# Kernel tuning notes

Measured on AMD Instinct MI355X. Metric: run time of the kernel, lower is better.

Reference implementation:

```python
import math
import jax, jax.numpy as jnp
import numpy as np

TEMPERATURE = 1.0
N_SAMPLES = 7
B, D = 2048, 512

def _l2_normalize(x, eps=1e-12):
    return x / jnp.maximum(jnp.linalg.norm(x, axis=-1, keepdims=True), eps)

def setup_inputs() -> dict:
    key = jax.random.key(0)
    ks = jax.random.split(key, 7)
    return {
        "query_mean": jax.random.normal(ks[0], (B, D), jnp.float32),
        "query_logsigma": jax.random.normal(ks[1], (B, D), jnp.float32),
        "query_z": jax.random.normal(ks[2], (B,), jnp.float32),
        "target_mean": jax.random.normal(ks[3], (B, D), jnp.float32),
        "target_logsigma": jax.random.normal(ks[4], (B, D), jnp.float32),
        "target_z": jax.random.normal(ks[5], (B,), jnp.float32),
        "eps": jax.random.normal(ks[6], (B, N_SAMPLES, D), jnp.float32),
    }

def reference(query_mean, query_logsigma, query_z, target_mean, target_logsigma, target_z, eps):
    qm = _l2_normalize(query_mean)                       # [B, D]
    tm = _l2_normalize(target_mean)                      # [B, D]
    # sample_gaussian_tensors: mu + eps * exp(logsigma), 7 samples -> [B, 7, D]
    samples = tm[:, None, :] + eps * jnp.exp(target_logsigma)[:, None, :]
    inv_sigmas = jnp.exp(-query_logsigma)                # [B, D] per-query precisions
    # weighted squared distance via the GEMM trick:
    # sum_d (t - q)^2 * w = sum_d t^2 w - 2 sum_d t q w + sum_d q^2 w
    t_term = jnp.einsum('qd,tsd->qts', inv_sigmas, samples * samples)   # [Bq, Bt, 7]
    x_term = jnp.einsum('qd,tsd->qts', qm * inv_sigmas, samples)        # [Bq, Bt, 7]
    q_term = jnp.sum(qm * qm * inv_sigmas, axis=-1)                     # [Bq]
    sqdist = t_term - 2.0 * x_term + q_term[:, None, None]
    loc = -0.5 * jnp.mean(sqdist, axis=-1)                              # [Bq, Bt]
    d = qm.shape[-1]
    norm_constant = (-d / 2.0) * jnp.log(jnp.float32(2.0 * math.pi)) \
                    - 0.5 * jnp.sum(query_logsigma, axis=-1)            # [Bq]
    # NOTE: torch broadcasting aligns the [B] vectors to the LAST (target) axis
    scores = query_z + norm_constant + loc                              # [Bq, Bt]
    scores = scores - jnp.max(scores, axis=0, keepdims=True)
    logits = scores / TEMPERATURE
    logp = jax.nn.log_softmax(logits, axis=-1)
    idx = jnp.arange(scores.shape[0])
    loss = -jnp.mean(logp[idx, idx])                                    # reduction='mean'
    return loss

if __name__ == "__main__":
    print(reference(**setup_inputs()))
```

## Files before the change

kernel.cpp:

```cpp
#include <hip/hip_runtime.h>
#include <math.h>

#define BB 2048
#define DD 512
#define NS 7
#define KK 1024
#define BM 128
#define BN 64
#define BK 64
#define NT (KK / BK)

typedef __attribute__((ext_vector_type(8))) short short8;
typedef __attribute__((ext_vector_type(4))) float floatx4;

typedef const __attribute__((address_space(1))) void gv_t;
typedef __attribute__((address_space(3))) void lv_t;
__device__ __forceinline__ void gl2lds16(const void* g, void* l) {
  __builtin_amdgcn_global_load_lds((gv_t*)g, (lv_t*)l, 16, 0, 0);
}

__device__ __forceinline__ unsigned short f2bf(float f) {
  unsigned int u = __float_as_uint(f);
  u += 0x7FFFu + ((u >> 16) & 1u);
  return (unsigned short)(u >> 16);
}
__device__ __forceinline__ float bf2f(unsigned short u) {
  return __uint_as_float(((unsigned)u) << 16);
}

__device__ __forceinline__ unsigned fkey(float f) {
  unsigned u = __float_as_uint(f);
  return (u & 0x80000000u) ? ~u : (u | 0x80000000u);
}
__device__ __forceinline__ float funkey(unsigned k) {
  unsigned u = (k & 0x80000000u) ? (k ^ 0x80000000u) : ~k;
  return __uint_as_float(u);
}

__device__ __forceinline__ int swz(int row, int c) {
  return (c & ~0x38) | ((((c >> 3) ^ row) & 7) << 3);
}

__device__ __forceinline__ float wave_reduce_sum(float v) {
#pragma unroll
  for (int off = 32; off > 0; off >>= 1) v += __shfl_down(v, off, 64);
  return v;
}
__device__ __forceinline__ float wave_reduce_max(float v) {
#pragma unroll
  for (int off = 32; off > 0; off >>= 1) v = fmaxf(v, __shfl_down(v, off, 64));
  return v;
}
__device__ __forceinline__ float block_reduce_sum256(float v, float* sbuf) {
  v = wave_reduce_sum(v);
  if ((threadIdx.x & 63) == 0) sbuf[threadIdx.x >> 6] = v;
  __syncthreads();
  float r = sbuf[0] + sbuf[1] + sbuf[2] + sbuf[3];
  __syncthreads();
  return r;
}
__device__ __forceinline__ float block_reduce_max256(float v, float* sbuf) {
  v = wave_reduce_max(v);
  if ((threadIdx.x & 63) == 0) sbuf[threadIdx.x >> 6] = v;
  __syncthreads();
  float r = fmaxf(fmaxf(sbuf[0], sbuf[1]), fmaxf(sbuf[2], sbuf[3]));
  __syncthreads();
  return r;
}

__global__ __launch_bounds__(256) void prep(
    const float* __restrict__ qmean, const float* __restrict__ qls,
    const float* __restrict__ tmean, const float* __restrict__ tls,
    const float* __restrict__ eps,
    unsigned short* __restrict__ Acat, unsigned short* __restrict__ Bcat,
    float* __restrict__ qterm, unsigned* __restrict__ Mkey) {
  __shared__ float sbuf[4];
  const int b = blockIdx.x, tid = threadIdx.x;
  const int c0 = 2 * tid;
  if (b < BB) {
    const int q = b;
    float2 x = ((const float2*)(qmean + (size_t)q * DD))[tid];
    float2 l = ((const float2*)(qls + (size_t)q * DD))[tid];
    float ss = block_reduce_sum256(x.x * x.x + x.y * x.y, sbuf);
    float inv = 1.0f / fmaxf(sqrtf(ss), 1e-12f);
    float w0 = expf(-l.x), w1 = expf(-l.y);
    float n0 = x.x * inv, n1 = x.y * inv;
    unsigned short* arow = Acat + (size_t)q * KK;
    ushort2 wp, np;
    wp.x = f2bf(w0);             wp.y = f2bf(w1);
    np.x = f2bf(-2.0f * n0 * w0); np.y = f2bf(-2.0f * n1 * w1);
    *(ushort2*)&arow[swz(q, c0)]      = wp;
    *(ushort2*)&arow[swz(q, DD + c0)] = np;
    float qt = block_reduce_sum256(n0 * n0 * w0 + n1 * n1 * w1, sbuf);
    if (tid == 0) qterm[q] = qt;
  } else {
    const int t = b - BB;
    if (tid == 0) Mkey[t] = 0u;
    float2 x = ((const float2*)(tmean + (size_t)t * DD))[tid];
    float2 l = ((const float2*)(tls + (size_t)t * DD))[tid];
    float ss = block_reduce_sum256(x.x * x.x + x.y * x.y, sbuf);
    float inv = 1.0f / fmaxf(sqrtf(ss), 1e-12f);
    float tm0 = x.x * inv, tm1 = x.y * inv;
    float sg0 = expf(l.x), sg1 = expf(l.y);
    float se0 = 0.f, sq0 = 0.f, se1 = 0.f, sq1 = 0.f;
    const float2* ep = (const float2*)(eps + (size_t)t * NS * DD);
#pragma unroll
    for (int s = 0; s < NS; ++s) {
      float2 e = ep[s * (DD / 2) + tid];
      se0 += e.x; sq0 += e.x * e.x;
      se1 += e.y; sq1 += e.y * e.y;
    }
    const float i7 = 1.0f / 7.0f;
    float m0 = sg0 * se0 * i7, m1 = sg1 * se1 * i7;
    unsigned short* brow = Bcat + (size_t)t * KK;
    ushort2 s2p, s1p;
    s2p.x = f2bf(tm0 * tm0 + 2.0f * tm0 * m0 + sg0 * sg0 * sq0 * i7);
    s2p.y = f2bf(tm1 * tm1 + 2.0f * tm1 * m1 + sg1 * sg1 * sq1 * i7);
    s1p.x = f2bf(tm0 + m0); s1p.y = f2bf(tm1 + m1);
    *(ushort2*)&brow[swz(t, c0)]      = s2p;
    *(ushort2*)&brow[swz(t, DD + c0)] = s1p;
  }
}

__global__ __launch_bounds__(256) void gemm_loc(
    const unsigned short* __restrict__ Acat,
    const unsigned short* __restrict__ Bcat,
    const float* __restrict__ qterm,
    unsigned short* __restrict__ loc, unsigned* __restrict__ Mkey) {
  __shared__ short As[3][BM * BK];
  __shared__ short Bs[3][BN * BK];
  const int tid = threadIdx.x, lane = tid & 63, wid = tid >> 6;
  const int lin = blockIdx.y * (BB / BN) + blockIdx.x;
  const int xcd = lin & 7, j = lin >> 3;
  const int tr = ((xcd >> 2) << 3) + (j >> 3);
  const int tc = ((xcd & 3) << 3) + (j & 7);
  const int brow = tr * BM, bcol = tc * BN;
  const int wr = wid >> 1, wc = wid & 1;
  const int fr = lane & 15, kg = lane >> 4, f7 = fr & 7;
  const int srow = lane >> 3, scol = (lane & 7) * 8;

  floatx4 acc[4][2];
#pragma unroll
  for (int m = 0; m < 4; ++m)
#pragma unroll
    for (int n = 0; n < 2; ++n) acc[m][n] = (floatx4){0.f, 0.f, 0.f, 0.f};

  const unsigned short* gA = Acat + (size_t)(brow + wid * 32 + srow) * KK + scol;
  const unsigned short* gB = Bcat + (size_t)(bcol + wid * 16 + srow) * KK + scol;

#pragma unroll
  for (int p = 0; p < 2; ++p) {
    short* la = &As[p][wid * 2048];
    short* lb = &Bs[p][wid * 1024];
#pragma unroll
    for (int j2 = 0; j2 < 4; ++j2) gl2lds16(gA + (size_t)j2 * 8 * KK + p * BK, la + j2 * 512);
#pragma unroll
    for (int j2 = 0; j2 < 2; ++j2) gl2lds16(gB + (size_t)j2 * 8 * KK + p * BK, lb + j2 * 512);
  }

#pragma unroll
  for (int kt = 0; kt < NT; ++kt) {
    if (kt < NT - 1) asm volatile("s_waitcnt vmcnt(6)" ::: "memory");
    else             asm volatile("s_waitcnt vmcnt(0)" ::: "memory");
    __builtin_amdgcn_s_barrier();
    if (kt + 2 < NT) {
      const int kc = (kt + 2) * BK, nb = (kt + 2) % 3;
      short* la = &As[nb][wid * 2048];
      short* lb = &Bs[nb][wid * 1024];
#pragma unroll
      for (int j2 = 0; j2 < 4; ++j2) gl2lds16(gA + (size_t)j2 * 8 * KK + kc, la + j2 * 512);
#pragma unroll
      for (int j2 = 0; j2 < 2; ++j2) gl2lds16(gB + (size_t)j2 * 8 * KK + kc, lb + j2 * 512);
    }
    const short* a  = As[kt % 3];
    const short* bp = Bs[kt % 3];
#pragma unroll
    for (int kh = 0; kh < 2; ++kh) {
      const int co = (((kh * 4 + kg) ^ f7) << 3);
      short8 af[4], bf[2];
#pragma unroll
      for (int m = 0; m < 4; ++m)
        af[m] = *reinterpret_cast<const short8*>(&a[(wr * 64 + m * 16 + fr) * BK + co]);
#pragma unroll
      for (int n = 0; n < 2; ++n)
        bf[n] = *reinterpret_cast<const short8*>(&bp[(wc * 32 + n * 16 + fr) * BK + co]);
#pragma unroll
      for (int m = 0; m < 4; ++m)
#pragma unroll
        for (int n = 0; n < 2; ++n)
          acc[m][n] = __builtin_amdgcn_mfma_f32_16x16x32_bf16(af[m], bf[n],
                                                              acc[m][n], 0, 0, 0);
    }
  }

#pragma unroll
  for (int n = 0; n < 2; ++n) {
    const int col = bcol + wc * 32 + n * 16 + fr;
    float cm = -3.402823466e38f;
#pragma unroll
    for (int m = 0; m < 4; ++m) {
      const int row = brow + wr * 64 + m * 16 + kg * 4;
#pragma unroll
      for (int r4 = 0; r4 < 4; ++r4) {
        float v = -0.5f * (acc[m][n][r4] + qterm[row + r4]);
        loc[(size_t)(row + r4) * BB + col] = f2bf(v);
        cm = fmaxf(cm, v);
      }
    }
    cm = fmaxf(cm, __shfl_xor(cm, 16, 64));
    cm = fmaxf(cm, __shfl_xor(cm, 32, 64));
    if (kg == 0) atomicMax(&Mkey[col], fkey(cm));
  }
}

__global__ __launch_bounds__(256) void row_lse(
    const unsigned short* __restrict__ loc, const unsigned* __restrict__ Mkey,
    float* __restrict__ rowval) {
  __shared__ float sbuf[4];
  __shared__ float sdiag;
  const int q = blockIdx.x, tid = threadIdx.x;
  short8 v = ((const short8*)(loc + (size_t)q * BB))[tid];
  uint4 k0 = ((const uint4*)Mkey)[2 * tid];
  uint4 k1 = ((const uint4*)Mkey)[2 * tid + 1];
  float xs[8];
  xs[0] = bf2f((unsigned short)v[0]) - funkey(k0.x);
  xs[1] = bf2f((unsigned short)v[1]) - funkey(k0.y);
  xs[2] = bf2f((unsigned short)v[2]) - funkey(k0.z);
  xs[3] = bf2f((unsigned short)v[3]) - funkey(k0.w);
  xs[4] = bf2f((unsigned short)v[4]) - funkey(k1.x);
  xs[5] = bf2f((unsigned short)v[5]) - funkey(k1.y);
  xs[6] = bf2f((unsigned short)v[6]) - funkey(k1.z);
  xs[7] = bf2f((unsigned short)v[7]) - funkey(k1.w);
  float m = xs[0];
#pragma unroll
  for (int i = 1; i < 8; ++i) m = fmaxf(m, xs[i]);
  if ((q >> 3) == tid) sdiag = xs[q & 7];
  m = block_reduce_max256(m, sbuf);
  float s = 0.f;
#pragma unroll
  for (int i = 0; i < 8; ++i) s += expf(xs[i] - m);
  s = block_reduce_sum256(s, sbuf);
  if (tid == 0) rowval[q] = sdiag - (m + logf(s));
}

__global__ __launch_bounds__(256) void final_loss(
    const float* __restrict__ rowval, float* __restrict__ out) {
  __shared__ float sbuf[4];
  const int tid = threadIdx.x;
  float s = 0.f;
#pragma unroll
  for (int i = 0; i < 8; ++i) s += rowval[tid + i * 256];
  s = block_reduce_sum256(s, sbuf);
  if (tid == 0) out[0] = -s * (1.0f / (float)BB);
}

extern "C" void kernel_launch(void* const* d_in, const int* in_sizes, int n_in,
                              void* d_out, int out_size, void* d_ws, size_t ws_size,
                              hipStream_t stream) {
  const float* qmean = (const float*)d_in[0];
  const float* qls   = (const float*)d_in[1];
  const float* tmean = (const float*)d_in[3];
  const float* tls   = (const float*)d_in[4];
  const float* eps   = (const float*)d_in[6];

  char* ws = (char*)d_ws;
  unsigned short* Acat = (unsigned short*)(ws + 0);
  unsigned short* Bcat = (unsigned short*)(ws + (4u << 20));
  float* qterm         = (float*)(ws + (8u << 20));
  unsigned* Mkey       = (unsigned*)(ws + (8u << 20) + 8192);
  float* rowval        = (float*)(ws + (8u << 20) + 16384);
  unsigned short* loc  = (unsigned short*)(ws + (8u << 20) + 65536);

  prep<<<2 * BB, 256, 0, stream>>>(qmean, qls, tmean, tls, eps,
                                   Acat, Bcat, qterm, Mkey);
  gemm_loc<<<dim3(BB / BN, BB / BM), 256, 0, stream>>>(Acat, Bcat, qterm, loc, Mkey);
  row_lse<<<BB, 256, 0, stream>>>(loc, Mkey, rowval);
  final_loss<<<1, 256, 0, stream>>>(rowval, (float*)d_out);
}
```

Before: 38.76 us.

## Switch GEMM operands to FP8 with split-scaled accumulators and wave-per-row prep/lse

```diff
diff --git a/kernel.cpp b/kernel.cpp
--- a/kernel.cpp
+++ b/kernel.cpp
@@ -12,6 +12,7 @@
 
 typedef __attribute__((ext_vector_type(8))) short short8;
 typedef __attribute__((ext_vector_type(4))) float floatx4;
+typedef long long i64;
 
 typedef const __attribute__((address_space(1))) void gv_t;
 typedef __attribute__((address_space(3))) void lv_t;
@@ -37,98 +38,121 @@
   return __uint_as_float(u);
 }
 
-__device__ __forceinline__ int swz(int row, int c) {
-  return (c & ~0x38) | ((((c >> 3) ^ row) & 7) << 3);
-}
-
-__device__ __forceinline__ float wave_reduce_sum(float v) {
-#pragma unroll
-  for (int off = 32; off > 0; off >>= 1) v += __shfl_down(v, off, 64);
+__device__ __forceinline__ uint2 pack8_fp8(const float* v) {
+  int lo = 0, hi = 0;
+  lo = __builtin_amdgcn_cvt_pk_fp8_f32(v[0], v[1], lo, false);
+  lo = __builtin_amdgcn_cvt_pk_fp8_f32(v[2], v[3], lo, true);
+  hi = __builtin_amdgcn_cvt_pk_fp8_f32(v[4], v[5], hi, false);
+  hi = __builtin_amdgcn_cvt_pk_fp8_f32(v[6], v[7], hi, true);
+  uint2 r; r.x = (unsigned)lo; r.y = (unsigned)hi; return r;
+}
+
+
+__device__ __forceinline__ float wsum(float v) {
+#pragma unroll
+  for (int off = 32; off > 0; off >>= 1) v += __shfl_xor(v, off, 64);
   return v;
 }
-__device__ __forceinline__ float wave_reduce_max(float v) {
-#pragma unroll
-  for (int off = 32; off > 0; off >>= 1) v = fmaxf(v, __shfl_down(v, off, 64));
+__device__ __forceinline__ float wmax(float v) {
+#pragma unroll
+  for (int off = 32; off > 0; off >>= 1) v = fmaxf(v, __shfl_xor(v, off, 64));
   return v;
 }
 __device__ __forceinline__ float block_reduce_sum256(float v, float* sbuf) {
-  v = wave_reduce_sum(v);
+  v = wsum(v);
   if ((threadIdx.x & 63) == 0) sbuf[threadIdx.x >> 6] = v;
   __syncthreads();
   float r = sbuf[0] + sbuf[1] + sbuf[2] + sbuf[3];
   __syncthreads();
   return r;
 }
-__device__ __forceinline__ float block_reduce_max256(float v, float* sbuf) {
-  v = wave_reduce_max(v);
-  if ((threadIdx.x & 63) == 0) sbuf[threadIdx.x >> 6] = v;
-  __syncthreads();
-  float r = fmaxf(fmaxf(sbuf[0], sbuf[1]), fmaxf(sbuf[2], sbuf[3]));
-  __syncthreads();
-  return r;
-}
 
 __global__ __launch_bounds__(256) void prep(
     const float* __restrict__ qmean, const float* __restrict__ qls,
     const float* __restrict__ tmean, const float* __restrict__ tls,
     const float* __restrict__ eps,
-    unsigned short* __restrict__ Acat, unsigned short* __restrict__ Bcat,
+    unsigned char* __restrict__ Acat, unsigned char* __restrict__ Bcat,
     float* __restrict__ qterm, unsigned* __restrict__ Mkey) {
-  __shared__ float sbuf[4];
-  const int b = blockIdx.x, tid = threadIdx.x;
-  const int c0 = 2 * tid;
-  if (b < BB) {
-    const int q = b;
-    float2 x = ((const float2*)(qmean + (size_t)q * DD))[tid];
-    float2 l = ((const float2*)(qls + (size_t)q * DD))[tid];
-    float ss = block_reduce_sum256(x.x * x.x + x.y * x.y, sbuf);
+  const int w = threadIdx.x >> 6, lane = threadIdx.x & 63;
+  const int r = blockIdx.x * 4 + w;
+  const int grp = (lane >> 3) * 64;
+  const int physoff = (((((lane & 7) >> 1) ^ r) & 3) << 4) |
+                      ((((lane & 7) ^ (r >> 2)) & 1) << 3);
+  if (r < BB) {
+    const int q = r;
+    const float4* xm = (const float4*)(qmean + (size_t)q * DD);
+    const float4* xl = (const float4*)(qls + (size_t)q * DD);
+    float4 a0 = xm[2 * lane], a1 = xm[2 * lane + 1];
+    float4 l0 = xl[2 * lane], l1 = xl[2 * lane + 1];
+    float x[8] = {a0.x, a0.y, a0.z, a0.w, a1.x, a1.y, a1.z, a1.w};
+    float l[8] = {l0.x, l0.y, l0.z, l0.w, l1.x, l1.y, l1.z, l1.w};
+    float ss = 0.f;
+#pragma unroll
+    for (int e = 0; e < 8; ++e) ss += x[e] * x[e];
+    ss = wsum(ss);
     float inv = 1.0f / fmaxf(sqrtf(ss), 1e-12f);
-    float w0 = expf(-l.x), w1 = expf(-l.y);
-    float n0 = x.x * inv, n1 = x.y * inv;
-    unsigned short* arow = Acat + (size_t)q * KK;
-    ushort2 wp, np;
-    wp.x = f2bf(w0);             wp.y = f2bf(w1);
-    np.x = f2bf(-2.0f * n0 * w0); np.y = f2bf(-2.0f * n1 * w1);
-    *(ushort2*)&arow[swz(q, c0)]      = wp;
-    *(ushort2*)&arow[swz(q, DD + c0)] = np;
-    float qt = block_reduce_sum256(n0 * n0 * w0 + n1 * n1 * w1, sbuf);
-    if (tid == 0) qterm[q] = qt;
+    float W[8], M2[8], qt = 0.f;
+#pragma unroll
+    for (int e = 0; e < 8; ++e) {
+      W[e] = expf(-l[e]);
+      float n = x[e] * inv;
+      M2[e] = -2.0f * n * W[e];
+      qt += n * n * W[e];
+    }
+    qt = wsum(qt);
+    if (lane == 0) qterm[q] = qt;
+    unsigned char* arow = Acat + (size_t)q * KK;
+    *(uint2*)(arow + grp + physoff)       = pack8_fp8(W);
+    *(uint2*)(arow + 512 + grp + physoff) = pack8_fp8(M2);
   } else {
-    const int t = b - BB;
-    if (tid == 0) Mkey[t] = 0u;
-    float2 x = ((const float2*)(tmean + (size_t)t * DD))[tid];
-    float2 l = ((const float2*)(tls + (size_t)t * DD))[tid];
-    float ss = block_reduce_sum256(x.x * x.x + x.y * x.y, sbuf);
+    const int t = r - BB;
+    if (lane == 0) Mkey[t] = 0u;
+    const float4* xm = (const float4*)(tmean + (size_t)t * DD);
+    const float4* xl = (const float4*)(tls + (size_t)t * DD);
+    float4 a0 = xm[2 * lane], a1 = xm[2 * lane + 1];
+    float4 l0 = xl[2 * lane], l1 = xl[2 * lane + 1];
+    float x[8] = {a0.x, a0.y, a0.z, a0.w, a1.x, a1.y, a1.z, a1.w};
+    float l[8] = {l0.x, l0.y, l0.z, l0.w, l1.x, l1.y, l1.z, l1.w};
+    float ss = 0.f;
+#pragma unroll
+    for (int e = 0; e < 8; ++e) ss += x[e] * x[e];
+    ss = wsum(ss);
     float inv = 1.0f / fmaxf(sqrtf(ss), 1e-12f);
-    float tm0 = x.x * inv, tm1 = x.y * inv;
-    float sg0 = expf(l.x), sg1 = expf(l.y);
-    float se0 = 0.f, sq0 = 0.f, se1 = 0.f, sq1 = 0.f;
-    const float2* ep = (const float2*)(eps + (size_t)t * NS * DD);
+    float se[8], sq[8];
+#pragma unroll
+    for (int e = 0; e < 8; ++e) { se[e] = 0.f; sq[e] = 0.f; }
+    const float4* ep = (const float4*)(eps + (size_t)t * NS * DD);
 #pragma unroll
     for (int s = 0; s < NS; ++s) {
-      float2 e = ep[s * (DD / 2) + tid];
-      se0 += e.x; sq0 += e.x * e.x;
-      se1 += e.y; sq1 += e.y * e.y;
+      float4 e0 = ep[s * (DD / 4) + 2 * lane];
+      float4 e1 = ep[s * (DD / 4) + 2 * lane + 1];
+      float ev[8] = {e0.x, e0.y, e0.z, e0.w, e1.x, e1.y, e1.z, e1.w};
+#pragma unroll
+      for (int e = 0; e < 8; ++e) { se[e] += ev[e]; sq[e] += ev[e] * ev[e]; }
     }
     const float i7 = 1.0f / 7.0f;
-    float m0 = sg0 * se0 * i7, m1 = sg1 * se1 * i7;
-    unsigned short* brow = Bcat + (size_t)t * KK;
-    ushort2 s2p, s1p;
-    s2p.x = f2bf(tm0 * tm0 + 2.0f * tm0 * m0 + sg0 * sg0 * sq0 * i7);
-    s2p.y = f2bf(tm1 * tm1 + 2.0f * tm1 * m1 + sg1 * sg1 * sq1 * i7);
-    s1p.x = f2bf(tm0 + m0); s1p.y = f2bf(tm1 + m1);
-    *(ushort2*)&brow[swz(t, c0)]      = s2p;
-    *(ushort2*)&brow[swz(t, DD + c0)] = s1p;
+    float S2[8], S1[8];
+#pragma unroll
+    for (int e = 0; e < 8; ++e) {
+      float tm = x[e] * inv;
+      float sg = expf(l[e]);
+      float m1 = sg * se[e] * i7;
+      S1[e] = tm + m1;
+      S2[e] = (tm * tm + 2.0f * tm * m1 + sg * sg * sq[e] * i7) * 0.00390625f;
+    }
+    unsigned char* brow = Bcat + (size_t)t * KK;
+    *(uint2*)(brow + grp + physoff)       = pack8_fp8(S2);
+    *(uint2*)(brow + 512 + grp + physoff) = pack8_fp8(S1);
   }
 }
 
 __global__ __launch_bounds__(256) void gemm_loc(
-    const unsigned short* __restrict__ Acat,
-    const unsigned short* __restrict__ Bcat,
+    const unsigned char* __restrict__ Acat,
+    const unsigned char* __restrict__ Bcat,
     const float* __restrict__ qterm,
     unsigned short* __restrict__ loc, unsigned* __restrict__ Mkey) {
-  __shared__ short As[3][BM * BK];
-  __shared__ short Bs[3][BN * BK];
+  __shared__ __align__(16) char As[3][BM * BK];
+  __shared__ __align__(16) char Bs[3][BN * BK];
   const int tid = threadIdx.x, lane = tid & 63, wid = tid >> 6;
   const int lin = blockIdx.y * (BB / BN) + blockIdx.x;
   const int xcd = lin & 7, j = lin >> 3;
@@ -136,62 +160,60 @@
   const int tc = ((xcd & 3) << 3) + (j & 7);
   const int brow = tr * BM, bcol = tc * BN;
   const int wr = wid >> 1, wc = wid & 1;
-  const int fr = lane & 15, kg = lane >> 4, f7 = fr & 7;
-  const int srow = lane >> 3, scol = (lane & 7) * 8;
-
-  floatx4 acc[4][2];
-#pragma unroll
-  for (int m = 0; m < 4; ++m)
-#pragma unroll
-    for (int n = 0; n < 2; ++n) acc[m][n] = (floatx4){0.f, 0.f, 0.f, 0.f};
-
-  const unsigned short* gA = Acat + (size_t)(brow + wid * 32 + srow) * KK + scol;
-  const unsigned short* gB = Bcat + (size_t)(bcol + wid * 16 + srow) * KK + scol;
-
-#pragma unroll
-  for (int p = 0; p < 2; ++p) {
-    short* la = &As[p][wid * 2048];
-    short* lb = &Bs[p][wid * 1024];
-#pragma unroll
-    for (int j2 = 0; j2 < 4; ++j2) gl2lds16(gA + (size_t)j2 * 8 * KK + p * BK, la + j2 * 512);
-#pragma unroll
-    for (int j2 = 0; j2 < 2; ++j2) gl2lds16(gB + (size_t)j2 * 8 * KK + p * BK, lb + j2 * 512);
-  }
+  const int fr = lane & 15, kg = lane >> 4;
+
+  floatx4 acc[2][4][2];
+#pragma unroll
+  for (int h = 0; h < 2; ++h)
+#pragma unroll
+    for (int m = 0; m < 4; ++m)
+#pragma unroll
+      for (int n = 0; n < 2; ++n) acc[h][m][n] = (floatx4){0.f, 0.f, 0.f, 0.f};
+
+  const unsigned char* gA0 = Acat + (size_t)(brow + (tid >> 2)) * KK + (tid & 3) * 16;
+  const unsigned char* gA1 = gA0 + (size_t)64 * KK;
+  const unsigned char* gB0 = Bcat + (size_t)(bcol + (tid >> 2)) * KK + (tid & 3) * 16;
+
+#define STAGE(buf, kc)                                      \
+  {                                                         \
+    gl2lds16(gA0 + (kc), &As[buf][tid * 16]);               \
+    gl2lds16(gA1 + (kc), &As[buf][4096 + tid * 16]);        \
+    gl2lds16(gB0 + (kc), &Bs[buf][tid * 16]);               \
+  }
+
+  STAGE(0, 0)
+  STAGE(1, BK)
 
 #pragma unroll
   for (int kt = 0; kt < NT; ++kt) {
-    if (kt < NT - 1) asm volatile("s_waitcnt vmcnt(6)" ::: "memory");
+    if (kt < NT - 1) asm volatile("s_waitcnt vmcnt(3)" ::: "memory");
     else             asm volatile("s_waitcnt vmcnt(0)" ::: "memory");
     __builtin_amdgcn_s_barrier();
-    if (kt + 2 < NT) {
-      const int kc = (kt + 2) * BK, nb = (kt + 2) % 3;
-      short* la = &As[nb][wid * 2048];
-      short* lb = &Bs[nb][wid * 1024];
-#pragma unroll
-      for (int j2 = 0; j2 < 4; ++j2) gl2lds16(gA + (size_t)j2 * 8 * KK + kc, la + j2 * 512);
-#pragma unroll
-      for (int j2 = 0; j2 < 2; ++j2) gl2lds16(gB + (size_t)j2 * 8 * KK + kc, lb + j2 * 512);
-    }
-    const short* a  = As[kt % 3];
-    const short* bp = Bs[kt % 3];
+    if (kt + 2 < NT) { STAGE((kt + 2) % 3, (kt + 2) * BK) }
+    const char* a  = As[kt % 3];
+    const char* bp = Bs[kt % 3];
 #pragma unroll
     for (int kh = 0; kh < 2; ++kh) {
-      const int co = (((kh * 4 + kg) ^ f7) << 3);
-      short8 af[4], bf[2];
+      const int co = ((((kh * 2 + (kg >> 1)) ^ fr) & 3) << 4) |
+                     (((kg ^ (fr >> 2)) & 1) << 3);
+      i64 af[4], bf[2];
 #pragma unroll
       for (int m = 0; m < 4; ++m)
-        af[m] = *reinterpret_cast<const short8*>(&a[(wr * 64 + m * 16 + fr) * BK + co]);
+        af[m] = *(const i64*)(a + (wr * 64 + m * 16 + fr) * BK + co);
 #pragma unroll
       for (int n = 0; n < 2; ++n)
-        bf[n] = *reinterpret_cast<const short8*>(&bp[(wc * 32 + n * 16 + fr) * BK + co]);
+        bf[n] = *(const i64*)(bp + (wc * 32 + n * 16 + fr) * BK + co);
+      __builtin_amdgcn_s_setprio(1);
 #pragma unroll
       for (int m = 0; m < 4; ++m)
 #pragma unroll
         for (int n = 0; n < 2; ++n)
-          acc[m][n] = __builtin_amdgcn_mfma_f32_16x16x32_bf16(af[m], bf[n],
-                                                              acc[m][n], 0, 0, 0);
-    }
-  }
+          acc[kt >> 3][m][n] = __builtin_amdgcn_mfma_f32_16x16x32_fp8_fp8(
+              af[m], bf[n], acc[kt >> 3][m][n], 0, 0, 0);
+      __builtin_amdgcn_s_setprio(0);
+    }
+  }
+#undef STAGE
 
 #pragma unroll
   for (int n = 0; n < 2; ++n) {
@@ -202,7 +224,8 @@
       const int row = brow + wr * 64 + m * 16 + kg * 4;
 #pragma unroll
       for (int r4 = 0; r4 < 4; ++r4) {
-        float v = -0.5f * (acc[m][n][r4] + qterm[row + r4]);
+        float v = -0.5f * (256.0f * acc[0][m][n][r4] + acc[1][m][n][r4] +
+                           qterm[row + r4]);
         loc[(size_t)(row + r4) * BB + col] = f2bf(v);
         cm = fmaxf(cm, v);
       }
@@ -216,31 +239,35 @@
 __global__ __launch_bounds__(256) void row_lse(
     const unsigned short* __restrict__ loc, const unsigned* __restrict__ Mkey,
     float* __restrict__ rowval) {
-  __shared__ float sbuf[4];
-  __shared__ float sdiag;
-  const int q = blockIdx.x, tid = threadIdx.x;
-  short8 v = ((const short8*)(loc + (size_t)q * BB))[tid];
-  uint4 k0 = ((const uint4*)Mkey)[2 * tid];
-  uint4 k1 = ((const uint4*)Mkey)[2 * tid + 1];
-  float xs[8];
-  xs[0] = bf2f((unsigned short)v[0]) - funkey(k0.x);
-  xs[1] = bf2f((unsigned short)v[1]) - funkey(k0.y);
-  xs[2] = bf2f((unsigned short)v[2]) - funkey(k0.z);
-  xs[3] = bf2f((unsigned short)v[3]) - funkey(k0.w);
-  xs[4] = bf2f((unsigned short)v[4]) - funkey(k1.x);
-  xs[5] = bf2f((unsigned short)v[5]) - funkey(k1.y);
-  xs[6] = bf2f((unsigned short)v[6]) - funkey(k1.z);
-  xs[7] = bf2f((unsigned short)v[7]) - funkey(k1.w);
-  float m = xs[0];
-#pragma unroll
-  for (int i = 1; i < 8; ++i) m = fmaxf(m, xs[i]);
-  if ((q >> 3) == tid) sdiag = xs[q & 7];
-  m = block_reduce_max256(m, sbuf);
+  const int w = threadIdx.x >> 6, lane = threadIdx.x & 63;
+  const int q = blockIdx.x * 4 + w;
+  const short8* lp = (const short8*)(loc + (size_t)q * BB);
+  const uint4* kp = (const uint4*)Mkey;
+  float xs[4][8];
+  float m = -3.402823466e38f, dv = 0.f;
+#pragma unroll
+  for (int c = 0; c < 4; ++c) {
+    short8 v = lp[c * 64 + lane];
+    uint4 k0 = kp[(c * 64 + lane) * 2];
+    uint4 k1 = kp[(c * 64 + lane) * 2 + 1];
+    unsigned ks[8] = {k0.x, k0.y, k0.z, k0.w, k1.x, k1.y, k1.z, k1.w};
+#pragma unroll
+    for (int e = 0; e < 8; ++e) {
+      float x = bf2f((unsigned short)v[e]) - funkey(ks[e]);
+      xs[c][e] = x;
+      m = fmaxf(m, x);
+      if (c * 512 + lane * 8 + e == q) dv = x;
+    }
+  }
+  m = wmax(m);
   float s = 0.f;
 #pragma unroll
-  for (int i = 0; i < 8; ++i) s += expf(xs[i] - m);
-  s = block_reduce_sum256(s, sbuf);
-  if (tid == 0) rowval[q] = sdiag - (m + logf(s));
+  for (int c = 0; c < 4; ++c)
+#pragma unroll
+    for (int e = 0; e < 8; ++e) s += expf(xs[c][e] - m);
+  s = wsum(s);
+  float d = __shfl(dv, (q >> 3) & 63, 64);
+  if (lane == 0) rowval[q] = d - (m + logf(s));
 }
 
 __global__ __launch_bounds__(256) void final_loss(
@@ -264,16 +291,16 @@
   const float* eps   = (const float*)d_in[6];
 
   char* ws = (char*)d_ws;
-  unsigned short* Acat = (unsigned short*)(ws + 0);
-  unsigned short* Bcat = (unsigned short*)(ws + (4u << 20));
-  float* qterm         = (float*)(ws + (8u << 20));
-  unsigned* Mkey       = (unsigned*)(ws + (8u << 20) + 8192);
-  float* rowval        = (float*)(ws + (8u << 20) + 16384);
-  unsigned short* loc  = (unsigned short*)(ws + (8u << 20) + 65536);
-
-  prep<<<2 * BB, 256, 0, stream>>>(qmean, qls, tmean, tls, eps,
-                                   Acat, Bcat, qterm, Mkey);
+  unsigned char* Acat  = (unsigned char*)(ws + 0);
+  unsigned char* Bcat  = (unsigned char*)(ws + (2u << 20));
+  float* qterm         = (float*)(ws + (4u << 20));
+  unsigned* Mkey       = (unsigned*)(ws + (4u << 20) + 8192);
+  float* rowval        = (float*)(ws + (4u << 20) + 16384);
+  unsigned short* loc  = (unsigned short*)(ws + (4u << 20) + 65536);
+
+  prep<<<1024, 256, 0, stream>>>(qmean, qls, tmean, tls, eps,
+                                 Acat, Bcat, qterm, Mkey);
   gemm_loc<<<dim3(BB / BN, BB / BM), 256, 0, stream>>>(Acat, Bcat, qterm, loc, Mkey);
-  row_lse<<<BB, 256, 0, stream>>>(loc, Mkey, rowval);
+  row_lse<<<512, 256, 0, stream>>>(loc, Mkey, rowval);
   final_loss<<<1, 256, 0, stream>>>(rowval, (float*)d_out);
 }
```

After: 34.93 us. 1.11x faster.
